# Kernel optimization log

Hardware: AMD Instinct MI355X
Metric: run time of the kernel (lower is better)

Reference implementation:

```python
import jax, jax.numpy as jnp
import numpy as np

B, T, C, H = 4, 2048, 768, 12
D = C // H  # head dim = 64

def setup_inputs() -> dict:
    key = jax.random.key(0)
    k1, k2, k3 = jax.random.split(key, 3)
    x = jax.random.normal(k1, (B, T, C), dtype=jnp.float32)
    W_attn = jax.random.normal(k2, (C, 3 * C), dtype=jnp.float32) * 0.02
    b_attn = jnp.zeros((3 * C,), dtype=jnp.float32)
    W_proj = jax.random.normal(k3, (C, C), dtype=jnp.float32) * 0.02
    b_proj = jnp.zeros((C,), dtype=jnp.float32)
    return {"x": x, "W_attn": W_attn, "b_attn": b_attn, "W_proj": W_proj, "b_proj": b_proj}

def reference(x, W_attn, b_attn, W_proj, b_proj):
    Bx, Tx, Cx = x.shape
    qkv = x @ W_attn + b_attn                      # [B,T,3C]
    q, k, v = jnp.split(qkv, 3, axis=2)
    q = q.reshape(Bx, Tx, H, D).swapaxes(1, 2)     # [B,H,T,D]
    k = k.reshape(Bx, Tx, H, D).swapaxes(1, 2)
    v = v.reshape(Bx, Tx, H, D).swapaxes(1, 2)
    att = jnp.einsum('bhqd,bhkd->bhqk', q, k) / jnp.sqrt(jnp.float32(D))
    mask = jnp.tril(jnp.ones((Tx, Tx), dtype=bool))
    att = jnp.where(mask, att, -jnp.inf)
    att = jax.nn.softmax(att, axis=-1)
    y = jnp.einsum('bhqk,bhkd->bhqd', att, v)      # [B,H,T,D]
    y = y.swapaxes(1, 2).reshape(Bx, Tx, Cx)
    return y @ W_proj + b_proj
```

## Files before the change

### kernel.cpp

```cpp
#include <hip/hip_runtime.h>
#include <hip/hip_bf16.h>

#define BATCH 4
#define TSEQ  2048
#define CDIM  768
#define HNUM  12
#define DHEAD 64
#define NQKV  (3*CDIM)
#define BTOT  (BATCH*TSEQ)
#define BH    (BATCH*HNUM)

typedef unsigned short u16;
typedef __attribute__((ext_vector_type(8))) __bf16 bf16x8;
typedef __attribute__((ext_vector_type(4))) float f32x4;

#define MFMA16(a,b,c) __builtin_amdgcn_mfma_f32_16x16x32_bf16((a),(b),(c),0,0,0)

__device__ __forceinline__ u16 f2b(float f) {
    union { float f; unsigned u; } v; v.f = f;
    unsigned u = v.u;
    unsigned r = (u + 0x7fffu + ((u >> 16) & 1u)) >> 16;
    return (u16)r;
}

__device__ __forceinline__ unsigned cvtpk(float lo, float hi) {
    unsigned r;
    asm("v_cvt_pk_bf16_f32 %0, %1, %2" : "=v"(r) : "v"(lo), "v"(hi));
    return r;
}

__device__ __forceinline__ float fexp2(float x) {
    float r;
    asm("v_exp_f32 %0, %1" : "=v"(r) : "v"(x));
    return r;
}

__device__ __forceinline__ void gload_lds(const void* g, void* l) {
    __builtin_amdgcn_global_load_lds(
        (const __attribute__((address_space(1))) void*)g,
        (__attribute__((address_space(3))) void*)l, 16, 0, 0);
}

__global__ __launch_bounds__(256) void cast_f32_bf16(
        const float* __restrict__ in, u16* __restrict__ out, int n4) {
    int i = blockIdx.x * blockDim.x + threadIdx.x;
    if (i >= n4) return;
    float4 a = reinterpret_cast<const float4*>(in)[i];
    ushort4 o;
    o.x = f2b(a.x); o.y = f2b(a.y); o.z = f2b(a.z); o.w = f2b(a.w);
    reinterpret_cast<ushort4*>(out)[i] = o;
}

__global__ __launch_bounds__(256) void tcast(
        const float* __restrict__ in, u16* __restrict__ out, int R, int Cc) {
    __shared__ float tile[32][33];
    int c0 = blockIdx.x * 32, r0 = blockIdx.y * 32;
    int tx = threadIdx.x, ty = threadIdx.y;
    #pragma unroll
    for (int i = 0; i < 32; i += 8)
        tile[ty + i][tx] = in[(size_t)(r0 + ty + i) * Cc + c0 + tx];
    __syncthreads();
    #pragma unroll
    for (int i = 0; i < 32; i += 8)
        out[(size_t)(c0 + ty + i) * R + r0 + tx] = f2b(tile[tx][ty + i]);
}

template<int MODE, int NX>
__global__ __launch_bounds__(256) void gemm_bt(
        const u16* __restrict__ A, const u16* __restrict__ Bt,
        const float* __restrict__ bias,
        u16* __restrict__ qb, u16* __restrict__ kb, u16* __restrict__ vtb,
        float* __restrict__ outf, int M, int N, int K) {
    __shared__ u16 sA[3][128 * 32];
    __shared__ u16 sB[3][128 * 32];
    const int tid = threadIdx.x;
    const int lane = tid & 63;
    const int w = tid >> 6;
    const int wr = w >> 1, wc = w & 1;
    const int cpx = gridDim.x >> 3;
    const int wg = ((int)blockIdx.x & 7) * cpx + ((int)blockIdx.x >> 3);
    const int bx = wg % NX, by = wg / NX;
    const int m0 = by * 128, n0 = bx * 128;

    f32x4 acc[4][4] = {};

    auto stage = [&](int buf, int kt) {
        #pragma unroll
        for (int i = 0; i < 2; ++i) {
            int chunk = i * 256 + tid;
            int row = chunk >> 2, c8 = chunk & 3;
            gload_lds(A  + (size_t)(m0 + row) * K + kt * 32 + c8 * 8, &sA[buf][chunk * 8]);
            gload_lds(Bt + (size_t)(n0 + row) * K + kt * 32 + c8 * 8, &sB[buf][chunk * 8]);
        }
    };

    const int KT = K / 32;
    stage(0, 0); stage(1, 1);
    for (int kt = 0; kt < KT; ++kt) {
        if (kt + 1 < KT) asm volatile("s_waitcnt vmcnt(4)" ::: "memory");
        else             asm volatile("s_waitcnt vmcnt(0)" ::: "memory");
        __builtin_amdgcn_s_barrier();
        if (kt + 2 < KT) stage((kt + 2) % 3, kt + 2);
        const u16* cA = sA[kt % 3];
        const u16* cB = sB[kt % 3];
        bf16x8 af[4], bfr[4];
        #pragma unroll
        for (int m = 0; m < 4; ++m)
            af[m] = *(const bf16x8*)&cA[(wr * 64 + m * 16 + (lane & 15)) * 32 + ((lane >> 4) << 3)];
        #pragma unroll
        for (int n = 0; n < 4; ++n)
            bfr[n] = *(const bf16x8*)&cB[(wc * 64 + n * 16 + (lane & 15)) * 32 + ((lane >> 4) << 3)];
        #pragma unroll
        for (int m = 0; m < 4; ++m)
            #pragma unroll
            for (int n = 0; n < 4; ++n)
                acc[m][n] = MFMA16(bfr[n], af[m], acc[m][n]);
    }

    if (MODE == 0) {
        const int which = n0 / CDIM;
        #pragma unroll
        for (int m = 0; m < 4; ++m) {
            const int rg = m0 + wr * 64 + m * 16 + (lane & 15);
            const int b = rg >> 11, t = rg & (TSEQ - 1);
            #pragma unroll
            for (int n = 0; n < 4; ++n) {
                const int cg = n0 + wc * 64 + n * 16 + ((lane >> 4) << 2);
                const int c  = cg - which * CDIM;
                const int h  = c >> 6, d = c & 63;
                const size_t bh = (size_t)(b * HNUM + h);
                const float4 bv = *(const float4*)&bias[cg];
                const float v0 = acc[m][n][0] + bv.x;
                const float v1 = acc[m][n][1] + bv.y;
                const float v2 = acc[m][n][2] + bv.z;
                const float v3 = acc[m][n][3] + bv.w;
                if (which == 0) {
                    const float s = 0.1803368801111243f;
                    ushort4 pv;
                    pv.x = f2b(v0 * s); pv.y = f2b(v1 * s);
                    pv.z = f2b(v2 * s); pv.w = f2b(v3 * s);
                    *(ushort4*)&qb[(bh * TSEQ + t) * DHEAD + d] = pv;
                } else if (which == 1) {
                    ushort4 pv;
                    pv.x = f2b(v0); pv.y = f2b(v1); pv.z = f2b(v2); pv.w = f2b(v3);
                    *(ushort4*)&kb[(bh * TSEQ + t) * DHEAD + d] = pv;
                } else {
                    vtb[(bh * DHEAD + d + 0) * TSEQ + t] = f2b(v0);
                    vtb[(bh * DHEAD + d + 1) * TSEQ + t] = f2b(v1);
                    vtb[(bh * DHEAD + d + 2) * TSEQ + t] = f2b(v2);
                    vtb[(bh * DHEAD + d + 3) * TSEQ + t] = f2b(v3);
                }
            }
        }
    } else {
        #pragma unroll
        for (int m = 0; m < 4; ++m) {
            const int rg = m0 + wr * 64 + m * 16 + (lane & 15);
            #pragma unroll
            for (int n = 0; n < 4; ++n) {
                const int cg = n0 + wc * 64 + n * 16 + ((lane >> 4) << 2);
                const float4 bv = *(const float4*)&bias[cg];
                float4 ov;
                ov.x = acc[m][n][0] + bv.x;
                ov.y = acc[m][n][1] + bv.y;
                ov.z = acc[m][n][2] + bv.z;
                ov.w = acc[m][n][3] + bv.w;
                *(float4*)&outf[(size_t)rg * CDIM + cg] = ov;
            }
        }
    }
}

__global__ __launch_bounds__(256, 4) void attn_fwd(
        const u16* __restrict__ qb, const u16* __restrict__ kb,
        const u16* __restrict__ vtb, u16* __restrict__ yb) {
    __shared__ u16 sK[2][64 * 64];
    __shared__ u16 sVt[2][64 * 64];
    const int qt = 31 - (int)(blockIdx.x / BH);
    const int bh = blockIdx.x % BH;
    const int b = bh / HNUM, h = bh % HNUM;
    const int tid = threadIdx.x, lane = tid & 63, w = tid >> 6;
    const int g = lane >> 4, lq = lane & 15;
    const int qlo = qt * 64 + w * 16;
    const u16* qbase = qb  + (size_t)bh * TSEQ * DHEAD;
    const u16* kbase = kb  + (size_t)bh * TSEQ * DHEAD;
    const u16* vbase = vtb + (size_t)bh * DHEAD * TSEQ;

    bf16x8 qf[2];
    #pragma unroll
    for (int ks = 0; ks < 2; ++ks)
        qf[ks] = *(const bf16x8*)&qbase[(size_t)(qlo + lq) * DHEAD + ks * 32 + g * 8];

    union { unsigned u[4]; bf16x8 v; } ones;
    #pragma unroll
    for (int i = 0; i < 4; ++i) ones.u[i] = 0x3f803f80u;

    f32x4 o[4] = {};
    f32x4 ls = {};
    float mx = -__builtin_inff();

    auto STAGE = [&](int buf, int kt) {
        const int k0 = kt << 6;
        #pragma unroll
        for (int i = 0; i < 2; ++i) {
            int chunk = i * 256 + tid;
            int srow = chunk >> 3;
            int cb = ((chunk & 7) << 4) ^ ((srow & 7) << 4);
            gload_lds(kbase + (size_t)(k0 + srow) * DHEAD + (cb >> 1), &sK[buf][chunk * 8]);
            gload_lds(vbase + (size_t)srow * TSEQ + k0 + (cb >> 1),    &sVt[buf][chunk * 8]);
        }
    };

    const int nk = qt + 1;
    STAGE(0, 0);
    __syncthreads();
    for (int kt = 0; kt < nk; ++kt) {
        const int k0 = kt << 6;
        if (kt + 1 < nk) STAGE((kt + 1) & 1, kt + 1);
        const u16* cK = sK[kt & 1];
        const u16* cV = sVt[kt & 1];
        f32x4 s[4];
        #pragma unroll
        for (int n = 0; n < 4; ++n) s[n] = f32x4{0.f, 0.f, 0.f, 0.f};
        __builtin_amdgcn_s_setprio(1);
        #pragma unroll
        for (int n = 0; n < 4; ++n) {
            #pragma unroll
            for (int ks = 0; ks < 2; ++ks) {
                int r = n * 16 + lq;
                int lb = (r * 128 + (ks * 32 + g * 8) * 2) ^ ((r & 7) << 4);
                bf16x8 kf = *(const bf16x8*)((const char*)cK + lb);
                s[n] = MFMA16(kf, qf[ks], s[n]);
            }
        }
        __builtin_amdgcn_s_setprio(0);
        if (k0 + 63 > qlo) {
            const int qa = qlo + lq;
            #pragma unroll
            for (int n = 0; n < 4; ++n)
                #pragma unroll
                for (int j = 0; j < 4; ++j)
                    if (k0 + n * 16 + g * 4 + j > qa) s[n][j] = -__builtin_inff();
        }
        float t0 = fmaxf(fmaxf(s[0][0], s[0][1]), fmaxf(s[0][2], s[0][3]));
        float t1 = fmaxf(fmaxf(s[1][0], s[1][1]), fmaxf(s[1][2], s[1][3]));
        float t2 = fmaxf(fmaxf(s[2][0], s[2][1]), fmaxf(s[2][2], s[2][3]));
        float t3 = fmaxf(fmaxf(s[3][0], s[3][1]), fmaxf(s[3][2], s[3][3]));
        float tmax = fmaxf(fmaxf(t0, t1), fmaxf(t2, t3));
        tmax = fmaxf(tmax, __shfl_xor(tmax, 16));
        tmax = fmaxf(tmax, __shfl_xor(tmax, 32));
        if (__any(tmax > mx + 8.0f)) {
            float mnew = fmaxf(mx, tmax);
            float sc = fexp2(mx - mnew);
            mx = mnew;
            #pragma unroll
            for (int j = 0; j < 4; ++j) {
                float scj = __shfl(sc, (lane & 48) | ((g << 2) + j));
                ls[j] *= scj;
                #pragma unroll
                for (int n = 0; n < 4; ++n) o[n][j] *= scj;
            }
        }
        #pragma unroll
        for (int n = 0; n < 4; ++n)
            #pragma unroll
            for (int j = 0; j < 4; ++j)
                s[n][j] = fexp2(s[n][j] - mx);
        unsigned apk[4], bpk[4];
        #pragma unroll
        for (int n = 0; n < 4; ++n) {
            apk[n] = cvtpk(s[n][0], s[n][1]);
            bpk[n] = cvtpk(s[n][2], s[n][3]);
        }
        const int s0l = lq + ((lane & 16) << 1);
        const bool hi = (lane & 32) != 0;
        #pragma unroll
        for (int ks = 0; ks < 2; ++ks) {
            unsigned A0  = (unsigned)__shfl((int)apk[2 * ks],     s0l);
            unsigned B0  = (unsigned)__shfl((int)bpk[2 * ks],     s0l);
            unsigned A1  = (unsigned)__shfl((int)apk[2 * ks + 1], s0l);
            unsigned B1  = (unsigned)__shfl((int)bpk[2 * ks + 1], s0l);
            unsigned A0h = (unsigned)__shfl((int)apk[2 * ks],     s0l + 16);
            unsigned B0h = (unsigned)__shfl((int)bpk[2 * ks],     s0l + 16);
            unsigned A1h = (unsigned)__shfl((int)apk[2 * ks + 1], s0l + 16);
            unsigned B1h = (unsigned)__shfl((int)bpk[2 * ks + 1], s0l + 16);
            union { unsigned u[4]; bf16x8 v; } pa;
            pa.u[0] = hi ? A1  : A0;
            pa.u[1] = hi ? B1  : B0;
            pa.u[2] = hi ? A1h : A0h;
            pa.u[3] = hi ? B1h : B0h;
            __builtin_amdgcn_s_setprio(1);
            #pragma unroll
            for (int n = 0; n < 4; ++n) {
                int d = n * 16 + lq;
                int lb = (d * 128 + (ks * 32 + g * 8) * 2) ^ ((d & 7) << 4);
                bf16x8 vf = *(const bf16x8*)((const char*)cV + lb);
                o[n] = MFMA16(pa.v, vf, o[n]);
            }
            ls = MFMA16(pa.v, ones.v, ls);
            __builtin_amdgcn_s_setprio(0);
        }
        __syncthreads();
    }

    #pragma unroll
    for (int j = 0; j < 4; ++j) {
        float inv = 1.f / ls[j];
        const int t = qlo + g * 4 + j;
        #pragma unroll
        for (int n = 0; n < 4; ++n) {
            const int c = h * DHEAD + n * 16 + lq;
            yb[((size_t)b * TSEQ + t) * CDIM + c] = f2b(o[n][j] * inv);
        }
    }
}

extern "C" void kernel_launch(void* const* d_in, const int* in_sizes, int n_in,
                              void* d_out, int out_size, void* d_ws, size_t ws_size,
                              hipStream_t stream) {
    const float* x      = (const float*)d_in[0];
    const float* W_attn = (const float*)d_in[1];
    const float* b_attn = (const float*)d_in[2];
    const float* W_proj = (const float*)d_in[3];
    const float* b_proj = (const float*)d_in[4];
    float* out = (float*)d_out;

    u16* ws = (u16*)d_ws;
    u16* xb     = ws;
    u16* yb     = xb;
    u16* WattnT = xb     + (size_t)BTOT * CDIM;
    u16* WprojT = WattnT + (size_t)NQKV * CDIM;
    u16* qb     = WprojT + (size_t)CDIM * CDIM;
    u16* kb     = qb     + (size_t)BH * TSEQ * DHEAD;
    u16* vtb    = kb     + (size_t)BH * TSEQ * DHEAD;

    int n4 = BTOT * CDIM / 4;
    cast_f32_bf16<<<(n4 + 255) / 256, 256, 0, stream>>>(x, xb, n4);
    tcast<<<dim3(NQKV / 32, CDIM / 32), dim3(32, 8), 0, stream>>>(W_attn, WattnT, CDIM, NQKV);
    tcast<<<dim3(CDIM / 32, CDIM / 32), dim3(32, 8), 0, stream>>>(W_proj, WprojT, CDIM, CDIM);

    gemm_bt<0, NQKV / 128><<<dim3((NQKV / 128) * (BTOT / 128)), 256, 0, stream>>>(
        xb, WattnT, b_attn, qb, kb, vtb, nullptr, BTOT, NQKV, CDIM);

    attn_fwd<<<dim3((TSEQ / 64) * BH), 256, 0, stream>>>(qb, kb, vtb, yb);

    gemm_bt<1, CDIM / 128><<<dim3((CDIM / 128) * (BTOT / 128)), 256, 0, stream>>>(
        yb, WprojT, b_proj, nullptr, nullptr, nullptr, out, BTOT, CDIM, CDIM);
}
```

Measured before the change: 144.2 us.

## Split QKV GEMM into dedicated 128x256 tile kernel with swizzled LDS

Separates the QKV projection into its own kernel using 128x256 output tiles, with each wave owning a 64-column slice across all 128 rows. Shared-memory tiles get an XOR swizzle to reduce bank conflicts, and the MFMA block runs at raised wave priority. The output projection keeps the original 128x128 kernel. The larger tile raises register and LDS use (launch bounds now allow 2 blocks per SM) and halves the number of QKV workgroups, which may reduce occupancy.

```diff
diff --git a/kernel.cpp b/kernel.cpp
--- a/kernel.cpp
+++ b/kernel.cpp
@@ -65,12 +65,109 @@
         out[(size_t)(c0 + ty + i) * R + r0 + tx] = f2b(tile[tx][ty + i]);
 }
 
-template<int MODE, int NX>
-__global__ __launch_bounds__(256) void gemm_bt(
+template<int NX>
+__global__ __launch_bounds__(256, 2) void gemm_qkv(
         const u16* __restrict__ A, const u16* __restrict__ Bt,
         const float* __restrict__ bias,
         u16* __restrict__ qb, u16* __restrict__ kb, u16* __restrict__ vtb,
-        float* __restrict__ outf, int M, int N, int K) {
+        int K) {
+    __shared__ u16 sA[3][128 * 32];
+    __shared__ u16 sB[3][256 * 32];
+    const int tid = threadIdx.x;
+    const int lane = tid & 63;
+    const int w = tid >> 6;
+    const int g = lane >> 4, lr = lane & 15;
+    const int cpx = gridDim.x >> 3;
+    const int wg = ((int)blockIdx.x & 7) * cpx + ((int)blockIdx.x >> 3);
+    const int bx = wg % NX, by = wg / NX;
+    const int m0 = by * 128, n0 = bx * 256;
+
+    f32x4 acc[8][4] = {};
+
+    auto stage = [&](int buf, int kt) {
+        #pragma unroll
+        for (int i = 0; i < 2; ++i) {
+            int c = i * 256 + tid, r = c >> 2, s = c & 3;
+            int c8 = s ^ ((r >> 1) & 3);
+            gload_lds(A + (size_t)(m0 + r) * K + kt * 32 + c8 * 8, &sA[buf][c * 8]);
+        }
+        #pragma unroll
+        for (int i = 0; i < 4; ++i) {
+            int c = i * 256 + tid, r = c >> 2, s = c & 3;
+            int c8 = s ^ ((r >> 1) & 3);
+            gload_lds(Bt + (size_t)(n0 + r) * K + kt * 32 + c8 * 8, &sB[buf][c * 8]);
+        }
+    };
+
+    const int KT = K / 32;
+    stage(0, 0); stage(1, 1);
+    for (int kt = 0; kt < KT; ++kt) {
+        if (kt + 1 < KT) asm volatile("s_waitcnt vmcnt(6)" ::: "memory");
+        else             asm volatile("s_waitcnt vmcnt(0)" ::: "memory");
+        __builtin_amdgcn_s_barrier();
+        if (kt + 2 < KT) stage((kt + 2) % 3, kt + 2);
+        const u16* cA = sA[kt % 3];
+        const u16* cB = sB[kt % 3];
+        bf16x8 af[8], bfr[4];
+        #pragma unroll
+        for (int m = 0; m < 8; ++m) {
+            int r = m * 16 + lr;
+            af[m] = *(const bf16x8*)&cA[r * 32 + ((g ^ ((r >> 1) & 3)) << 3)];
+        }
+        #pragma unroll
+        for (int n = 0; n < 4; ++n) {
+            int r = w * 64 + n * 16 + lr;
+            bfr[n] = *(const bf16x8*)&cB[r * 32 + ((g ^ ((r >> 1) & 3)) << 3)];
+        }
+        __builtin_amdgcn_s_setprio(1);
+        #pragma unroll
+        for (int m = 0; m < 8; ++m)
+            #pragma unroll
+            for (int n = 0; n < 4; ++n)
+                acc[m][n] = MFMA16(bfr[n], af[m], acc[m][n]);
+        __builtin_amdgcn_s_setprio(0);
+    }
+
+    const int which = n0 / CDIM;
+    #pragma unroll
+    for (int m = 0; m < 8; ++m) {
+        const int rg = m0 + m * 16 + lr;
+        const int b = rg >> 11, t = rg & (TSEQ - 1);
+        #pragma unroll
+        for (int n = 0; n < 4; ++n) {
+            const int cg = n0 + w * 64 + n * 16 + (g << 2);
+            const int c  = cg - which * CDIM;
+            const int h  = c >> 6, d = c & 63;
+            const size_t bh = (size_t)(b * HNUM + h);
+            const float4 bv = *(const float4*)&bias[cg];
+            const float v0 = acc[m][n][0] + bv.x;
+            const float v1 = acc[m][n][1] + bv.y;
+            const float v2 = acc[m][n][2] + bv.z;
+            const float v3 = acc[m][n][3] + bv.w;
+            if (which == 0) {
+                const float s = 0.1803368801111243f;
+                ushort4 pv;
+                pv.x = f2b(v0 * s); pv.y = f2b(v1 * s);
+                pv.z = f2b(v2 * s); pv.w = f2b(v3 * s);
+                *(ushort4*)&qb[(bh * TSEQ + t) * DHEAD + d] = pv;
+            } else if (which == 1) {
+                ushort4 pv;
+                pv.x = f2b(v0); pv.y = f2b(v1); pv.z = f2b(v2); pv.w = f2b(v3);
+                *(ushort4*)&kb[(bh * TSEQ + t) * DHEAD + d] = pv;
+            } else {
+                vtb[(bh * DHEAD + d + 0) * TSEQ + t] = f2b(v0);
+                vtb[(bh * DHEAD + d + 1) * TSEQ + t] = f2b(v1);
+                vtb[(bh * DHEAD + d + 2) * TSEQ + t] = f2b(v2);
+                vtb[(bh * DHEAD + d + 3) * TSEQ + t] = f2b(v3);
+            }
+        }
+    }
+}
+
+template<int NX>
+__global__ __launch_bounds__(256) void gemm_out(
+        const u16* __restrict__ A, const u16* __restrict__ Bt,
+        const float* __restrict__ bias, float* __restrict__ outf, int K) {
     __shared__ u16 sA[3][128 * 32];
     __shared__ u16 sB[3][128 * 32];
     const int tid = threadIdx.x;
@@ -117,56 +214,19 @@
                 acc[m][n] = MFMA16(bfr[n], af[m], acc[m][n]);
     }
 
-    if (MODE == 0) {
-        const int which = n0 / CDIM;
-        #pragma unroll
-        for (int m = 0; m < 4; ++m) {
-            const int rg = m0 + wr * 64 + m * 16 + (lane & 15);
-            const int b = rg >> 11, t = rg & (TSEQ - 1);
-            #pragma unroll
-            for (int n = 0; n < 4; ++n) {
-                const int cg = n0 + wc * 64 + n * 16 + ((lane >> 4) << 2);
-                const int c  = cg - which * CDIM;
-                const int h  = c >> 6, d = c & 63;
-                const size_t bh = (size_t)(b * HNUM + h);
-                const float4 bv = *(const float4*)&bias[cg];
-                const float v0 = acc[m][n][0] + bv.x;
-                const float v1 = acc[m][n][1] + bv.y;
-                const float v2 = acc[m][n][2] + bv.z;
-                const float v3 = acc[m][n][3] + bv.w;
-                if (which == 0) {
-                    const float s = 0.1803368801111243f;
-                    ushort4 pv;
-                    pv.x = f2b(v0 * s); pv.y = f2b(v1 * s);
-                    pv.z = f2b(v2 * s); pv.w = f2b(v3 * s);
-                    *(ushort4*)&qb[(bh * TSEQ + t) * DHEAD + d] = pv;
-                } else if (which == 1) {
-                    ushort4 pv;
-                    pv.x = f2b(v0); pv.y = f2b(v1); pv.z = f2b(v2); pv.w = f2b(v3);
-                    *(ushort4*)&kb[(bh * TSEQ + t) * DHEAD + d] = pv;
-                } else {
-                    vtb[(bh * DHEAD + d + 0) * TSEQ + t] = f2b(v0);
-                    vtb[(bh * DHEAD + d + 1) * TSEQ + t] = f2b(v1);
-                    vtb[(bh * DHEAD + d + 2) * TSEQ + t] = f2b(v2);
-                    vtb[(bh * DHEAD + d + 3) * TSEQ + t] = f2b(v3);
-                }
-            }
-        }
-    } else {
-        #pragma unroll
-        for (int m = 0; m < 4; ++m) {
-            const int rg = m0 + wr * 64 + m * 16 + (lane & 15);
-            #pragma unroll
-            for (int n = 0; n < 4; ++n) {
-                const int cg = n0 + wc * 64 + n * 16 + ((lane >> 4) << 2);
-                const float4 bv = *(const float4*)&bias[cg];
-                float4 ov;
-                ov.x = acc[m][n][0] + bv.x;
-                ov.y = acc[m][n][1] + bv.y;
-                ov.z = acc[m][n][2] + bv.z;
-                ov.w = acc[m][n][3] + bv.w;
-                *(float4*)&outf[(size_t)rg * CDIM + cg] = ov;
-            }
+    #pragma unroll
+    for (int m = 0; m < 4; ++m) {
+        const int rg = m0 + wr * 64 + m * 16 + (lane & 15);
+        #pragma unroll
+        for (int n = 0; n < 4; ++n) {
+            const int cg = n0 + wc * 64 + n * 16 + ((lane >> 4) << 2);
+            const float4 bv = *(const float4*)&bias[cg];
+            float4 ov;
+            ov.x = acc[m][n][0] + bv.x;
+            ov.y = acc[m][n][1] + bv.y;
+            ov.z = acc[m][n][2] + bv.z;
+            ov.w = acc[m][n][3] + bv.w;
+            *(float4*)&outf[(size_t)rg * CDIM + cg] = ov;
         }
     }
 }
@@ -339,11 +399,11 @@
     tcast<<<dim3(NQKV / 32, CDIM / 32), dim3(32, 8), 0, stream>>>(W_attn, WattnT, CDIM, NQKV);
     tcast<<<dim3(CDIM / 32, CDIM / 32), dim3(32, 8), 0, stream>>>(W_proj, WprojT, CDIM, CDIM);
 
-    gemm_bt<0, NQKV / 128><<<dim3((NQKV / 128) * (BTOT / 128)), 256, 0, stream>>>(
-        xb, WattnT, b_attn, qb, kb, vtb, nullptr, BTOT, NQKV, CDIM);
+    gemm_qkv<NQKV / 256><<<dim3((NQKV / 256) * (BTOT / 128)), 256, 0, stream>>>(
+        xb, WattnT, b_attn, qb, kb, vtb, CDIM);
 
     attn_fwd<<<dim3((TSEQ / 64) * BH), 256, 0, stream>>>(qb, kb, vtb, yb);
 
-    gemm_bt<1, CDIM / 128><<<dim3((CDIM / 128) * (BTOT / 128)), 256, 0, stream>>>(
-        yb, WprojT, b_proj, nullptr, nullptr, nullptr, out, BTOT, CDIM, CDIM);
-}
+    gemm_out<CDIM / 128><<<dim3((CDIM / 128) * (BTOT / 128)), 256, 0, stream>>>(
+        yb, WprojT, b_proj, out, CDIM);
+}
```

New measurement: 152.3 us. 1.06x slower.
